# Kernel tuning notes

Hardware: AMD Instinct MI355X
Metric: run time of the kernel (lower is better)

## Reference

```python
import jax, jax.numpy as jnp
import numpy as np

B, S, D, H = 8, 2048, 1024, 8
CHUNK = D // H
SCALE = float(D) ** (-0.5)  # key_dim ** -0.5, key_dim == num_units here
LN_EPS = 1e-5


def setup_inputs() -> dict:
    key = jax.random.key(0)
    ks = jax.random.split(key, 9)
    s = 0.02
    return {
        "query": jax.random.normal(ks[0], (B, S, D), jnp.float32),
        "keys": jax.random.normal(ks[1], (B, S, D), jnp.float32),
        "Wq": jax.random.normal(ks[2], (D, D), jnp.float32) * s,  # torch Linear weight [out,in]
        "Wk": jax.random.normal(ks[3], (D, D), jnp.float32) * s,
        "Wv": jax.random.normal(ks[4], (D, D), jnp.float32) * s,
        "Wp": jax.random.normal(ks[5], (D, D), jnp.float32) * s,
        "bp": jnp.zeros((D,), jnp.float32),
        "ln_gamma": jnp.ones((D,), jnp.float32),
        "ln_beta": jnp.zeros((D,), jnp.float32),
    }


def reference(query, keys, Wq, Wk, Wv, Wp, bp, ln_gamma, ln_beta):
    # Linear layers (no bias on q/k/v): y = x @ W.T
    Q = jnp.einsum("bsd,ed->bse", query, Wq)
    K = jnp.einsum("bsd,ed->bse", keys, Wk)
    V = jnp.einsum("bsd,ed->bse", keys, Wv)
    # Faithful to original: raw view to [B*h, S, chunk] (no transpose head split)
    Qh = Q.reshape(B * H, S, CHUNK)
    Kh = K.reshape(B * H, S, CHUNK)
    Vh = V.reshape(B * H, S, CHUNK)
    # scores [B*h, S, S], scale, softmax (is_masked=False, dropout_p=0)
    att = jnp.einsum("gqc,gkc->gqk", Qh, Kh) * SCALE
    att = jax.nn.softmax(att, axis=-1)
    ctx = jnp.einsum("gqk,gkc->gqc", att, Vh).reshape(B, S, D)
    # output projection + residual + LayerNorm
    out = jnp.einsum("bsd,ed->bse", ctx, Wp) + bp
    out = out + query
    mu = jnp.mean(out, axis=-1, keepdims=True)
    var = jnp.mean(jnp.square(out - mu), axis=-1, keepdims=True)
    out = (out - mu) * jax.lax.rsqrt(var + LN_EPS) * ln_gamma + ln_beta
    return out
```

## Files before the change

### kernel.cpp

```cpp
#include <hip/hip_runtime.h>

typedef __bf16 bf16x8 __attribute__((ext_vector_type(8)));
typedef float f32x4 __attribute__((ext_vector_type(4)));

#define SCLOG 0.04508422f

__device__ __forceinline__ unsigned short f2bf(float f) {
  union { float f; unsigned int u; } v;
  v.f = f;
  unsigned int u = v.u;
  u += 0x7fffu + ((u >> 16) & 1u);
  return (unsigned short)(u >> 16);
}

__device__ __forceinline__ unsigned asuint(float f) {
  union { float f; unsigned u; } v; v.f = f; return v.u;
}

__device__ __forceinline__ void gld_lds16(const void* g, void* l) {
  __builtin_amdgcn_global_load_lds(
      (const __attribute__((address_space(1))) void*)g,
      (__attribute__((address_space(3))) void*)l, 16, 0, 0);
}

__global__ __launch_bounds__(256) void convert_kernel(
    const float* __restrict__ q, const float* __restrict__ k,
    const float* __restrict__ wq, const float* __restrict__ wk,
    const float* __restrict__ wv, const float* __restrict__ wp,
    unsigned short* __restrict__ qb, unsigned short* __restrict__ kb,
    unsigned short* __restrict__ Wqkv, unsigned short* __restrict__ Wpb) {
  size_t i = (size_t)blockIdx.x * 256 + threadIdx.x;
  const float* src; unsigned short* dst; size_t off;
  if (i < 4194304)      { src = q;  dst = qb;             off = i; }
  else if (i < 8388608) { src = k;  dst = kb;             off = i - 4194304; }
  else if (i < 8650752) { src = wq; dst = Wqkv;           off = i - 8388608; }
  else if (i < 8912896) { src = wk; dst = Wqkv + 1048576; off = i - 8650752; }
  else if (i < 9175040) { src = wv; dst = Wqkv + 2097152; off = i - 8912896; }
  else                  { src = wp; dst = Wpb;            off = i - 9175040; }
  float4 v = ((const float4*)src)[off];
  ushort4 o;
  o.x = f2bf(v.x); o.y = f2bf(v.y); o.z = f2bf(v.z); o.w = f2bf(v.w);
  ((ushort4*)dst)[off] = o;
}

#define QKV_BAR __builtin_amdgcn_s_barrier()
#define QKV_LGKM asm volatile("s_waitcnt lgkmcnt(0)" ::: "memory")

#define QKV_STG(lc, h, srcb, s)                                               \
  gld_lds16((srcb) + (size_t)(s) * 128 + gro0, (lc) + (h) * 16384 + d0);      \
  gld_lds16((srcb) + (size_t)(s) * 128 + gro1, (lc) + (h) * 16384 + d0 + 1024);

#define QKV_RDA(I0)                                                           \
  _Pragma("unroll") for (int i4 = 0; i4 < 4; ++i4) {                          \
    af[i4][0] = *(const bf16x8*)(tb + rbA + ((I0) + i4) * 2048 + cx0);        \
    af[i4][1] = *(const bf16x8*)(tb + rbA + ((I0) + i4) * 2048 + cx1);        \
  }

#define QKV_RDB(JP)                                                           \
  _Pragma("unroll") for (int j2 = 0; j2 < 2; ++j2) {                          \
    bfr[JP][j2][0] = *(const bf16x8*)(tb + rbB + ((JP) * 2 + j2) * 2048 + cx0); \
    bfr[JP][j2][1] = *(const bf16x8*)(tb + rbB + ((JP) * 2 + j2) * 2048 + cx1); \
  }

#define QKV_MM(I0, JP)                                                        \
  _Pragma("unroll") for (int i4 = 0; i4 < 4; ++i4)                            \
  _Pragma("unroll") for (int j2 = 0; j2 < 2; ++j2)                            \
  _Pragma("unroll") for (int kk = 0; kk < 2; ++kk)                            \
    acc[(I0) + i4][(JP) * 2 + j2] = __builtin_amdgcn_mfma_f32_16x16x32_bf16(  \
        af[i4][kk], bfr[JP][j2][kk], acc[(I0) + i4][(JP) * 2 + j2], 0, 0, 0);

__global__ __launch_bounds__(512, 2) void gemm_qkv8_kernel(
    const unsigned short* __restrict__ qb,
    const unsigned short* __restrict__ kb,
    const unsigned short* __restrict__ W,
    unsigned short* __restrict__ Qo,
    unsigned short* __restrict__ Ko,
    unsigned short* __restrict__ Vo) {
  __shared__ char lds[131072];

  const int t = threadIdx.x;
  const int lane = t & 63;
  const int w = t >> 6;
  const int fr = lane & 15;
  const int quad = lane >> 4;

  const int orig = blockIdx.x;
  const int sseq = orig >> 3;
  const int tn = sseq >> 3;
  const int tm = (orig & 7) * 8 + (sseq & 7);

  const unsigned short* Ap = (tn < 4) ? qb : kb;
  const char* aBase = (const char*)Ap + (size_t)(tm * 256) * 2048;
  const char* bBase = (const char*)W + (size_t)(tn * 256) * 2048;

  const int wm2 = w >> 2, wn4 = w & 3;

  const size_t gro0 = (size_t)(w * 16 + (lane >> 3)) * 2048 + (size_t)(((lane & 7) ^ (lane >> 3)) << 4);
  const size_t gro1 = gro0 + 8 * 2048;
  const int d0 = w * 2048 + lane * 16;

  const int rbA = (wm2 * 128 + fr) * 128;
  const int rbB = 32768 + (wn4 * 64 + fr) * 128;
  const int cx0 = (quad * 16) ^ ((fr & 7) << 4);
  const int cx1 = cx0 ^ 64;

  f32x4 acc[8][4];
#pragma unroll
  for (int i = 0; i < 8; ++i)
#pragma unroll
    for (int j = 0; j < 4; ++j) acc[i][j] = (f32x4){0.f, 0.f, 0.f, 0.f};

#pragma unroll
  for (int s = 0; s < 2; ++s) {
    char* lc = lds + s * 65536;
    QKV_STG(lc, 0, aBase, s);
    QKV_STG(lc, 1, aBase + 262144, s);
    QKV_STG(lc + 32768, 0, bBase, s);
    QKV_STG(lc + 32768, 1, bBase + 262144, s);
  }
  asm volatile("s_waitcnt vmcnt(8)" ::: "memory");
  QKV_BAR;

#pragma unroll 1
  for (int kt = 0; kt < 16; ++kt) {
    const char* tb = lds + (kt & 1) * 65536;
    char* lc = lds + (kt & 1) * 65536;
    const int s = kt + 2;
    bf16x8 af[4][2], bfr[2][2][2];

    QKV_RDA(0);
    QKV_RDB(0);
    QKV_BAR; QKV_LGKM;
    __builtin_amdgcn_s_setprio(1);
    QKV_MM(0, 0);
    __builtin_amdgcn_s_setprio(0);
    QKV_BAR;

    QKV_RDB(1);
    QKV_BAR; QKV_LGKM;
    __builtin_amdgcn_s_setprio(1);
    QKV_MM(0, 1);
    __builtin_amdgcn_s_setprio(0);
    QKV_BAR;

    QKV_RDA(4);
    if (s < 16) {
      QKV_STG(lc + 32768, 0, bBase, s);
      QKV_STG(lc + 32768, 1, bBase + 262144, s);
    }
    QKV_BAR; QKV_LGKM;
    __builtin_amdgcn_s_setprio(1);
    QKV_MM(4, 1);
    __builtin_amdgcn_s_setprio(0);
    QKV_BAR;

    if (s < 16) {
      QKV_STG(lc, 0, aBase, s);
      QKV_STG(lc, 1, aBase + 262144, s);
    }
    QKV_BAR;
    __builtin_amdgcn_s_setprio(1);
    QKV_MM(4, 0);
    __builtin_amdgcn_s_setprio(0);
    if (kt <= 13)      { asm volatile("s_waitcnt vmcnt(8)" ::: "memory"); }
    else if (kt == 14) { asm volatile("s_waitcnt vmcnt(0)" ::: "memory"); }
    if (kt < 15) QKV_BAR;
  }

  const int sel = tn >> 2;
  unsigned short* Out = sel == 0 ? Qo : (sel == 1 ? Ko : Vo);
  const int row0 = tm * 256 + wm2 * 128 + quad * 4;
  const int col0 = (tn & 3) * 256 + wn4 * 64 + fr;
#pragma unroll
  for (int i = 0; i < 8; ++i)
#pragma unroll
    for (int j = 0; j < 4; ++j)
#pragma unroll
      for (int r = 0; r < 4; ++r)
        Out[(size_t)(row0 + i * 16 + r) * 1024 + col0 + j * 16] = f2bf(acc[i][j][r]);
}

__global__ __launch_bounds__(256) void vtrans_kernel(
    const unsigned short* __restrict__ V, unsigned short* __restrict__ Vt) {
  __shared__ unsigned short T[128 * 136];
  const int g  = blockIdx.x >> 4;
  const int kt = blockIdx.x & 15;
  const unsigned short* Vg = V + (size_t)g * 262144 + (size_t)kt * 128 * 128;
  unsigned short* Vtg = Vt + (size_t)g * 262144 + kt * 128;
  const int t = threadIdx.x;
#pragma unroll
  for (int it = 0; it < 8; it++) {
    int seg = t + it * 256;
    int k  = seg >> 4;
    int c8 = (seg & 15) << 3;
    uint4 a = *(const uint4*)(Vg + k * 128 + c8);
    unsigned short* Tp = &T[c8 * 136 + k];
    Tp[0 * 136] = (unsigned short)(a.x & 0xffff);
    Tp[1 * 136] = (unsigned short)(a.x >> 16);
    Tp[2 * 136] = (unsigned short)(a.y & 0xffff);
    Tp[3 * 136] = (unsigned short)(a.y >> 16);
    Tp[4 * 136] = (unsigned short)(a.z & 0xffff);
    Tp[5 * 136] = (unsigned short)(a.z >> 16);
    Tp[6 * 136] = (unsigned short)(a.w & 0xffff);
    Tp[7 * 136] = (unsigned short)(a.w >> 16);
  }
  __syncthreads();
#pragma unroll
  for (int it = 0; it < 8; it++) {
    int seg = t + it * 256;
    int c  = seg >> 4;
    int k8 = (seg & 15) << 3;
    uint4 o = *(const uint4*)&T[c * 136 + k8];
    *(uint4*)(Vtg + (size_t)c * 2048 + k8) = o;
  }
}

__global__ __launch_bounds__(256, 2) void attn_kernel(
    const unsigned short* __restrict__ Q,
    const unsigned short* __restrict__ K,
    const unsigned short* __restrict__ Vt,
    unsigned short* __restrict__ ctx) {
  __shared__ unsigned char smem[81920];
  unsigned char* Psh = smem + 65536;

  const int g  = blockIdx.x >> 4;
  const int qt = blockIdx.x & 15;
  const unsigned short* Qg = Q + (size_t)g * 262144 + (size_t)qt * 16384;
  const unsigned short* Kg = K + (size_t)g * 262144;
  const unsigned short* Vg = Vt + (size_t)g * 262144;

  const int t    = threadIdx.x;
  const int lane = t & 63;
  const int wv   = t >> 6;
  const int fr   = lane & 15;
  const int quad = lane >> 4;

#pragma unroll
  for (int it = 0; it < 8; it++) {
    int seg = t + it * 256;
    int r = seg >> 4, p = seg & 15;
    int c = (p & 8) | ((p ^ r) & 7);
    gld_lds16(Qg + r * 128 + c * 8, smem + seg * 16);
  }
  __syncthreads();
  bf16x8 qf[2][4];
#pragma unroll
  for (int nt = 0; nt < 2; nt++)
#pragma unroll
    for (int kc = 0; kc < 4; kc++) {
      int row = wv * 32 + nt * 16 + fr;
      int c = kc * 4 + quad;
      int p = (c & 8) | ((c ^ (row & 7)) & 7);
      qf[nt][kc] = *(const bf16x8*)(smem + row * 256 + p * 16);
    }
  __syncthreads();

#pragma unroll
  for (int it = 0; it < 4; it++) {
    int seg = t + it * 256;
    int r = seg >> 4, p = seg & 15;
    int c = (p & 8) | ((p ^ r) & 7);
    gld_lds16(Kg + (size_t)r * 128 + c * 8, smem + seg * 16);
  }
#pragma unroll
  for (int it = 0; it < 4; it++) {
    int seg = t + it * 256;
    int r = seg >> 3, p = seg & 7;
    int c = p ^ (r & 7);
    gld_lds16(Vg + (size_t)r * 2048 + c * 8, smem + 32768 + seg * 16);
  }
  __syncthreads();

  f32x4 O[2][8];
#pragma unroll
  for (int qb2 = 0; qb2 < 2; qb2++)
#pragma unroll
    for (int cb = 0; cb < 8; cb++) O[qb2][cb] = (f32x4){0.f, 0.f, 0.f, 0.f};
  float lp[2] = {0.f, 0.f};

#pragma unroll 1
  for (int kt = 0; kt < 32; kt++) {
    unsigned char* Ksh = smem + (unsigned)(kt & 1) * 16384;
    unsigned char* Vsh = smem + 32768 + (unsigned)(kt & 1) * 16384;

    if (kt < 31) {
      unsigned char* Kst = smem + (unsigned)((kt + 1) & 1) * 16384;
      unsigned char* Vst = smem + 32768 + (unsigned)((kt + 1) & 1) * 16384;
#pragma unroll
      for (int it = 0; it < 4; it++) {
        int seg = t + it * 256;
        int r = seg >> 4, p = seg & 15;
        int c = (p & 8) | ((p ^ r) & 7);
        gld_lds16(Kg + (size_t)((kt + 1) * 64 + r) * 128 + c * 8, Kst + seg * 16);
      }
#pragma unroll
      for (int it = 0; it < 4; it++) {
        int seg = t + it * 256;
        int r = seg >> 3, p = seg & 7;
        int c = p ^ (r & 7);
        gld_lds16(Vg + (size_t)r * 2048 + (kt + 1) * 64 + c * 8, Vst + seg * 16);
      }
    }

#pragma unroll
    for (int mt = 0; mt < 4; mt++) {
      bf16x8 kf[4];
#pragma unroll
      for (int kc = 0; kc < 4; kc++) {
        int row = mt * 16 + fr;
        int c = kc * 4 + quad;
        int p = (c & 8) | ((c ^ (row & 7)) & 7);
        kf[kc] = *(const bf16x8*)(Ksh + row * 256 + p * 16);
      }
#pragma unroll
      for (int nt = 0; nt < 2; nt++) {
        f32x4 s = (f32x4){0.f, 0.f, 0.f, 0.f};
#pragma unroll
        for (int kc = 0; kc < 4; kc++)
          s = __builtin_amdgcn_mfma_f32_16x16x32_bf16(kf[kc], qf[nt][kc], s, 0, 0, 0);
        float p0 = exp2f(fminf(s[0] * SCLOG, 30.f));
        float p1 = exp2f(fminf(s[1] * SCLOG, 30.f));
        float p2 = exp2f(fminf(s[2] * SCLOG, 30.f));
        float p3 = exp2f(fminf(s[3] * SCLOG, 30.f));
        lp[nt] += (p0 + p1) + (p2 + p3);
        unsigned u01 = __builtin_amdgcn_perm(asuint(p1) + 0x8000u, asuint(p0) + 0x8000u, 0x07060302u);
        unsigned u23 = __builtin_amdgcn_perm(asuint(p3) + 0x8000u, asuint(p2) + 0x8000u, 0x07060302u);
        int qrow = wv * 32 + nt * 16 + fr;
        int cP = mt * 2 + (quad >> 1);
        int pP = cP ^ (qrow & 7);
        uint2 u2; u2.x = u01; u2.y = u23;
        *(uint2*)(Psh + qrow * 128 + pP * 16 + (quad & 1) * 8) = u2;
      }
    }

    bf16x8 pf[2][2];
#pragma unroll
    for (int qb2 = 0; qb2 < 2; qb2++)
#pragma unroll
      for (int k2 = 0; k2 < 2; k2++) {
        int qrow = wv * 32 + qb2 * 16 + fr;
        int c = k2 * 4 + quad;
        int p = c ^ (qrow & 7);
        pf[qb2][k2] = *(const bf16x8*)(Psh + qrow * 128 + p * 16);
      }
#pragma unroll
    for (int cb = 0; cb < 8; cb++)
#pragma unroll
      for (int k2 = 0; k2 < 2; k2++) {
        int crow = cb * 16 + fr;
        int c = k2 * 4 + quad;
        int p = c ^ (crow & 7);
        bf16x8 vf = *(const bf16x8*)(Vsh + crow * 128 + p * 16);
#pragma unroll
        for (int qb2 = 0; qb2 < 2; qb2++)
          O[qb2][cb] = __builtin_amdgcn_mfma_f32_16x16x32_bf16(pf[qb2][k2], vf, O[qb2][cb], 0, 0, 0);
      }

    __syncthreads();
  }

  float* linv_arr = (float*)(smem + 65536);
#pragma unroll
  for (int nt = 0; nt < 2; nt++) {
    float v = lp[nt];
    v += __shfl_xor(v, 16);
    v += __shfl_xor(v, 32);
    if (quad == 0) linv_arr[wv * 32 + nt * 16 + fr] = 1.f / v;
  }
  unsigned short* Cg = ctx + (size_t)g * 262144 + (size_t)qt * 16384;
#pragma unroll
  for (int qb2 = 0; qb2 < 2; qb2++) {
    float li[4];
#pragma unroll
    for (int r = 0; r < 4; r++) li[r] = linv_arr[wv * 32 + qb2 * 16 + quad * 4 + r];
#pragma unroll
    for (int cb = 0; cb < 8; cb++)
#pragma unroll
      for (int r = 0; r < 4; r++) {
        int qrow = wv * 32 + qb2 * 16 + quad * 4 + r;
        Cg[(size_t)qrow * 128 + cb * 16 + fr] = f2bf(O[qb2][cb][r] * li[r]);
      }
  }
}

__global__ __launch_bounds__(256) void gemm_proj_kernel(
    const unsigned short* __restrict__ A,
    const unsigned short* __restrict__ W,
    const float* __restrict__ bp,
    const float* __restrict__ qres,
    float* __restrict__ out) {
  __shared__ unsigned short Alds[128 * 32];
  __shared__ unsigned short Blds[128 * 32];
  const int t   = threadIdx.x;
  const int bid = blockIdx.x;
  const int tn  = bid % 8;
  const int tm  = bid / 8;
  const unsigned short* Bptr = W + (size_t)tn * 128 * 1024;

  const int lane = t & 63;
  const int wv   = t >> 6;
  const int wm   = (wv >> 1) * 64;
  const int wn   = (wv & 1) * 64;
  const int fr   = lane & 15;
  const int kq   = (lane >> 4) * 8;

  f32x4 acc[4][4];
#pragma unroll
  for (int i = 0; i < 4; i++)
#pragma unroll
    for (int j = 0; j < 4; j++) acc[i][j] = (f32x4){0.f, 0.f, 0.f, 0.f};

  const int sr = t >> 2;
  const int sc = (t & 3) << 3;
  const unsigned short* gA = A + (size_t)(tm * 128 + sr) * 1024 + sc;
  const unsigned short* gB = Bptr + (size_t)sr * 1024 + sc;
  unsigned short* lA = Alds + t * 8;
  unsigned short* lB = Blds + t * 8;

  for (int k0 = 0; k0 < 1024; k0 += 32) {
    gld_lds16(gA, lA);
    gld_lds16(gA + 64 * 1024, lA + 64 * 32);
    gld_lds16(gB, lB);
    gld_lds16(gB + 64 * 1024, lB + 64 * 32);
    gA += 32; gB += 32;
    __syncthreads();
    bf16x8 af[4], bfr[4];
#pragma unroll
    for (int i = 0; i < 4; i++) {
      af[i]  = *(const bf16x8*)&Alds[(wm + i * 16 + fr) * 32 + kq];
      bfr[i] = *(const bf16x8*)&Blds[(wn + i * 16 + fr) * 32 + kq];
    }
#pragma unroll
    for (int i = 0; i < 4; i++)
#pragma unroll
      for (int j = 0; j < 4; j++)
        acc[i][j] = __builtin_amdgcn_mfma_f32_16x16x32_bf16(af[i], bfr[j], acc[i][j], 0, 0, 0);
    __syncthreads();
  }

  const int quad = lane >> 4;
  const int cc   = lane & 15;
#pragma unroll
  for (int i = 0; i < 4; i++)
#pragma unroll
    for (int j = 0; j < 4; j++)
#pragma unroll
      for (int r = 0; r < 4; r++) {
        int row = tm * 128 + wm + i * 16 + quad * 4 + r;
        int col = tn * 128 + wn + j * 16 + cc;
        out[(size_t)row * 1024 + col] =
            acc[i][j][r] + bp[col] + qres[(size_t)row * 1024 + col];
      }
}

__global__ __launch_bounds__(256) void ln_kernel(float* __restrict__ out,
                                                 const float* __restrict__ gamma,
                                                 const float* __restrict__ beta) {
  __shared__ float red[8];
  const int row = blockIdx.x;
  float* p = out + (size_t)row * 1024;
  const int t = threadIdx.x;
  float4 v = ((const float4*)p)[t];
  float s  = v.x + v.y + v.z + v.w;
  float s2 = v.x * v.x + v.y * v.y + v.z * v.z + v.w * v.w;
#pragma unroll
  for (int off = 1; off < 64; off <<= 1) {
    s  += __shfl_xor(s, off);
    s2 += __shfl_xor(s2, off);
  }
  const int wv = t >> 6;
  if ((t & 63) == 0) { red[wv] = s; red[4 + wv] = s2; }
  __syncthreads();
  float S  = red[0] + red[1] + red[2] + red[3];
  float S2 = red[4] + red[5] + red[6] + red[7];
  float mu  = S * (1.f / 1024.f);
  float var = S2 * (1.f / 1024.f) - mu * mu;
  float rstd = rsqrtf(var + 1e-5f);
  float4 gm = ((const float4*)gamma)[t];
  float4 bt = ((const float4*)beta)[t];
  v.x = (v.x - mu) * rstd * gm.x + bt.x;
  v.y = (v.y - mu) * rstd * gm.y + bt.y;
  v.z = (v.z - mu) * rstd * gm.z + bt.z;
  v.w = (v.w - mu) * rstd * gm.w + bt.w;
  ((float4*)p)[t] = v;
}

extern "C" void kernel_launch(void* const* d_in, const int* in_sizes, int n_in,
                              void* d_out, int out_size, void* d_ws, size_t ws_size,
                              hipStream_t stream) {
  const float* query = (const float*)d_in[0];
  const float* keys  = (const float*)d_in[1];
  const float* Wq    = (const float*)d_in[2];
  const float* Wk    = (const float*)d_in[3];
  const float* Wv    = (const float*)d_in[4];
  const float* Wp    = (const float*)d_in[5];
  const float* bp    = (const float*)d_in[6];
  const float* gamma = (const float*)d_in[7];
  const float* beta  = (const float*)d_in[8];
  float* out = (float*)d_out;

  unsigned short* ws   = (unsigned short*)d_ws;
  unsigned short* qb   = ws;
  unsigned short* kb   = ws + 16777216;
  unsigned short* Wqkv = ws + 33554432;
  unsigned short* Wpb  = ws + 36700160;
  unsigned short* Qb   = ws + 37748736;
  unsigned short* Kb   = ws + 54525952;
  unsigned short* Vb   = ws + 71303168;
  unsigned short* Vtb  = kb;
  unsigned short* ctx  = qb;

  convert_kernel<<<36864, 256, 0, stream>>>(query, keys, Wq, Wk, Wv, Wp, qb, kb, Wqkv, Wpb);
  gemm_qkv8_kernel<<<768, 512, 0, stream>>>(qb, kb, Wqkv, Qb, Kb, Vb);
  vtrans_kernel<<<1024, 256, 0, stream>>>(Vb, Vtb);
  attn_kernel<<<1024, 256, 0, stream>>>(Qb, Kb, Vtb, ctx);
  gemm_proj_kernel<<<1024, 256, 0, stream>>>(ctx, Wpb, bp, query, out);
  ln_kernel<<<16384, 256, 0, stream>>>(out, gamma, beta);
}
```

Before: 565.4 us.

## Split attention block into eight waves of sixteen query rows each

Doubles the attention block to 512 threads, so each wave owns 16 query rows instead of 32. Per-wave Q fragments, O accumulators and row sums are halved, which cuts register use and allows more resident waves per CU to hide MFMA and exp latency. The price is that each K and V fragment is now read from LDS by twice as many waves, roughly doubling LDS read traffic per tile. The K/V staging loops are retuned for 512 threads.

```diff
diff --git a/kernel.cpp b/kernel.cpp
--- a/kernel.cpp
+++ b/kernel.cpp
@@ -215,7 +215,7 @@
   }
 }
 
-__global__ __launch_bounds__(256, 2) void attn_kernel(
+__global__ __launch_bounds__(512, 4) void attn_kernel(
     const unsigned short* __restrict__ Q,
     const unsigned short* __restrict__ K,
     const unsigned short* __restrict__ Vt,
@@ -236,47 +236,43 @@
   const int quad = lane >> 4;
 
 #pragma unroll
-  for (int it = 0; it < 8; it++) {
-    int seg = t + it * 256;
+  for (int it = 0; it < 4; it++) {
+    int seg = t + it * 512;
     int r = seg >> 4, p = seg & 15;
     int c = (p & 8) | ((p ^ r) & 7);
     gld_lds16(Qg + r * 128 + c * 8, smem + seg * 16);
   }
   __syncthreads();
-  bf16x8 qf[2][4];
-#pragma unroll
-  for (int nt = 0; nt < 2; nt++)
-#pragma unroll
-    for (int kc = 0; kc < 4; kc++) {
-      int row = wv * 32 + nt * 16 + fr;
-      int c = kc * 4 + quad;
-      int p = (c & 8) | ((c ^ (row & 7)) & 7);
-      qf[nt][kc] = *(const bf16x8*)(smem + row * 256 + p * 16);
-    }
+  bf16x8 qf[4];
+#pragma unroll
+  for (int kc = 0; kc < 4; kc++) {
+    int row = wv * 16 + fr;
+    int c = kc * 4 + quad;
+    int p = (c & 8) | ((c ^ (row & 7)) & 7);
+    qf[kc] = *(const bf16x8*)(smem + row * 256 + p * 16);
+  }
   __syncthreads();
 
 #pragma unroll
-  for (int it = 0; it < 4; it++) {
-    int seg = t + it * 256;
+  for (int it = 0; it < 2; it++) {
+    int seg = t + it * 512;
     int r = seg >> 4, p = seg & 15;
     int c = (p & 8) | ((p ^ r) & 7);
     gld_lds16(Kg + (size_t)r * 128 + c * 8, smem + seg * 16);
   }
 #pragma unroll
-  for (int it = 0; it < 4; it++) {
-    int seg = t + it * 256;
+  for (int it = 0; it < 2; it++) {
+    int seg = t + it * 512;
     int r = seg >> 3, p = seg & 7;
     int c = p ^ (r & 7);
     gld_lds16(Vg + (size_t)r * 2048 + c * 8, smem + 32768 + seg * 16);
   }
   __syncthreads();
 
-  f32x4 O[2][8];
-#pragma unroll
-  for (int qb2 = 0; qb2 < 2; qb2++)
-#pragma unroll
-    for (int cb = 0; cb < 8; cb++) O[qb2][cb] = (f32x4){0.f, 0.f, 0.f, 0.f};
-  float lp[2] = {0.f, 0.f};
+  f32x4 O[8];
+#pragma unroll
+  for (int cb = 0; cb < 8; cb++) O[cb] = (f32x4){0.f, 0.f, 0.f, 0.f};
+  float lp = 0.f;
 
 #pragma unroll 1
   for (int kt = 0; kt < 32; kt++) {
@@ -287,15 +283,15 @@
       unsigned char* Kst = smem + (unsigned)((kt + 1) & 1) * 16384;
       unsigned char* Vst = smem + 32768 + (unsigned)((kt + 1) & 1) * 16384;
 #pragma unroll
-      for (int it = 0; it < 4; it++) {
-        int seg = t + it * 256;
+      for (int it = 0; it < 2; it++) {
+        int seg = t + it * 512;
         int r = seg >> 4, p = seg & 15;
         int c = (p & 8) | ((p ^ r) & 7);
         gld_lds16(Kg + (size_t)((kt + 1) * 64 + r) * 128 + c * 8, Kst + seg * 16);
       }
 #pragma unroll
-      for (int it = 0; it < 4; it++) {
-        int seg = t + it * 256;
+      for (int it = 0; it < 2; it++) {
+        int seg = t + it * 512;
         int r = seg >> 3, p = seg & 7;
         int c = p ^ (r & 7);
         gld_lds16(Vg + (size_t)r * 2048 + (kt + 1) * 64 + c * 8, Vst + seg * 16);
@@ -312,37 +308,32 @@
         int p = (c & 8) | ((c ^ (row & 7)) & 7);
         kf[kc] = *(const bf16x8*)(Ksh + row * 256 + p * 16);
       }
-#pragma unroll
-      for (int nt = 0; nt < 2; nt++) {
-        f32x4 s = (f32x4){0.f, 0.f, 0.f, 0.f};
-#pragma unroll
-        for (int kc = 0; kc < 4; kc++)
-          s = __builtin_amdgcn_mfma_f32_16x16x32_bf16(kf[kc], qf[nt][kc], s, 0, 0, 0);
-        float p0 = exp2f(fminf(s[0] * SCLOG, 30.f));
-        float p1 = exp2f(fminf(s[1] * SCLOG, 30.f));
-        float p2 = exp2f(fminf(s[2] * SCLOG, 30.f));
-        float p3 = exp2f(fminf(s[3] * SCLOG, 30.f));
-        lp[nt] += (p0 + p1) + (p2 + p3);
-        unsigned u01 = __builtin_amdgcn_perm(asuint(p1) + 0x8000u, asuint(p0) + 0x8000u, 0x07060302u);
-        unsigned u23 = __builtin_amdgcn_perm(asuint(p3) + 0x8000u, asuint(p2) + 0x8000u, 0x07060302u);
-        int qrow = wv * 32 + nt * 16 + fr;
-        int cP = mt * 2 + (quad >> 1);
-        int pP = cP ^ (qrow & 7);
-        uint2 u2; u2.x = u01; u2.y = u23;
-        *(uint2*)(Psh + qrow * 128 + pP * 16 + (quad & 1) * 8) = u2;
-      }
-    }
-
-    bf16x8 pf[2][2];
-#pragma unroll
-    for (int qb2 = 0; qb2 < 2; qb2++)
-#pragma unroll
-      for (int k2 = 0; k2 < 2; k2++) {
-        int qrow = wv * 32 + qb2 * 16 + fr;
-        int c = k2 * 4 + quad;
-        int p = c ^ (qrow & 7);
-        pf[qb2][k2] = *(const bf16x8*)(Psh + qrow * 128 + p * 16);
-      }
+      f32x4 s = (f32x4){0.f, 0.f, 0.f, 0.f};
+#pragma unroll
+      for (int kc = 0; kc < 4; kc++)
+        s = __builtin_amdgcn_mfma_f32_16x16x32_bf16(kf[kc], qf[kc], s, 0, 0, 0);
+      float p0 = exp2f(fminf(s[0] * SCLOG, 30.f));
+      float p1 = exp2f(fminf(s[1] * SCLOG, 30.f));
+      float p2 = exp2f(fminf(s[2] * SCLOG, 30.f));
+      float p3 = exp2f(fminf(s[3] * SCLOG, 30.f));
+      lp += (p0 + p1) + (p2 + p3);
+      unsigned u01 = __builtin_amdgcn_perm(asuint(p1) + 0x8000u, asuint(p0) + 0x8000u, 0x07060302u);
+      unsigned u23 = __builtin_amdgcn_perm(asuint(p3) + 0x8000u, asuint(p2) + 0x8000u, 0x07060302u);
+      int qrow = wv * 16 + fr;
+      int cP = mt * 2 + (quad >> 1);
+      int pP = cP ^ (qrow & 7);
+      uint2 u2; u2.x = u01; u2.y = u23;
+      *(uint2*)(Psh + qrow * 128 + pP * 16 + (quad & 1) * 8) = u2;
+    }
+
+    bf16x8 pf[2];
+#pragma unroll
+    for (int k2 = 0; k2 < 2; k2++) {
+      int qrow = wv * 16 + fr;
+      int c = k2 * 4 + quad;
+      int p = c ^ (qrow & 7);
+      pf[k2] = *(const bf16x8*)(Psh + qrow * 128 + p * 16);
+    }
 #pragma unroll
     for (int cb = 0; cb < 8; cb++)
 #pragma unroll
@@ -351,36 +342,30 @@
         int c = k2 * 4 + quad;
         int p = c ^ (crow & 7);
         bf16x8 vf = *(const bf16x8*)(Vsh + crow * 128 + p * 16);
-#pragma unroll
-        for (int qb2 = 0; qb2 < 2; qb2++)
-          O[qb2][cb] = __builtin_amdgcn_mfma_f32_16x16x32_bf16(pf[qb2][k2], vf, O[qb2][cb], 0, 0, 0);
+        O[cb] = __builtin_amdgcn_mfma_f32_16x16x32_bf16(pf[k2], vf, O[cb], 0, 0, 0);
       }
 
     __syncthreads();
   }
 
   float* linv_arr = (float*)(smem + 65536);
-#pragma unroll
-  for (int nt = 0; nt < 2; nt++) {
-    float v = lp[nt];
+  {
+    float v = lp;
     v += __shfl_xor(v, 16);
     v += __shfl_xor(v, 32);
-    if (quad == 0) linv_arr[wv * 32 + nt * 16 + fr] = 1.f / v;
+    if (quad == 0) linv_arr[wv * 16 + fr] = 1.f / v;
   }
   unsigned short* Cg = ctx + (size_t)g * 262144 + (size_t)qt * 16384;
-#pragma unroll
-  for (int qb2 = 0; qb2 < 2; qb2++) {
-    float li[4];
-#pragma unroll
-    for (int r = 0; r < 4; r++) li[r] = linv_arr[wv * 32 + qb2 * 16 + quad * 4 + r];
-#pragma unroll
-    for (int cb = 0; cb < 8; cb++)
-#pragma unroll
-      for (int r = 0; r < 4; r++) {
-        int qrow = wv * 32 + qb2 * 16 + quad * 4 + r;
-        Cg[(size_t)qrow * 128 + cb * 16 + fr] = f2bf(O[qb2][cb][r] * li[r]);
-      }
-  }
+  float li[4];
+#pragma unroll
+  for (int r = 0; r < 4; r++) li[r] = linv_arr[wv * 16 + quad * 4 + r];
+#pragma unroll
+  for (int cb = 0; cb < 8; cb++)
+#pragma unroll
+    for (int r = 0; r < 4; r++) {
+      int qrow = wv * 16 + quad * 4 + r;
+      Cg[(size_t)qrow * 128 + cb * 16 + fr] = f2bf(O[cb][r] * li[r]);
+    }
 }
 
 __global__ __launch_bounds__(256) void gemm_proj_kernel(
@@ -513,7 +498,7 @@
   convert_kernel<<<36864, 256, 0, stream>>>(query, keys, Wq, Wk, Wv, Wp, qb, kb, Wqkv, Wpb);
   gemm_qkv8_kernel<<<768, 512, 0, stream>>>(qb, kb, Wqkv, Qb, Kb, Vb);
   vtrans_kernel<<<1024, 256, 0, stream>>>(Vb, Vtb);
-  attn_kernel<<<1024, 256, 0, stream>>>(Qb, Kb, Vtb, ctx);
+  attn_kernel<<<1024, 512, 0, stream>>>(Qb, Kb, Vtb, ctx);
   gemm_proj_kernel<<<1024, 256, 0, stream>>>(ctx, Wpb, bp, query, out);
   ln_kernel<<<16384, 256, 0, stream>>>(out, gamma, beta);
 }
```

New measurement: 564.5 us. No clear change (-0.2%).
